# Kernel tuning notes

Measured on AMD Instinct MI355X. Metric: run time of the kernel, lower is better.

## Reference

```python
import jax, jax.numpy as jnp
import numpy as np

N_NODES = 50000
N_EDGES = 400000
IN_DIM = 256
HIDDEN = 256
HEADS = 8
DPH = HIDDEN // HEADS  # 32, out_per_head
OUT_DIM = 128
SEG_EPS = 1e-12   # eps in _segment_softmax
BN_EPS = 1e-5     # torch BatchNorm1d default eps


def _xavier(key, shape):
    fan_in, fan_out = shape[0], shape[-1]
    lim = np.sqrt(6.0 / (fan_in + fan_out))
    return jax.random.uniform(key, shape, jnp.float32, -lim, lim)


def setup_inputs() -> dict:
    key = jax.random.key(0)
    ks = jax.random.split(key, 16)
    x = jax.random.normal(ks[0], (N_NODES, IN_DIM), jnp.float32)
    edge_index = jax.random.randint(ks[1], (2, N_EDGES), 0, N_NODES, jnp.int64)
    return {
        "x": x,
        "edge_index": edge_index,
        # layer 1
        "W1": _xavier(ks[2], (IN_DIM, HIDDEN)),
        "b1": jnp.zeros((HIDDEN,), jnp.float32),
        "a_l1": _xavier(ks[3], (HEADS, DPH)),
        "a_r1": _xavier(ks[4], (HEADS, DPH)),
        "g1": jnp.ones((HIDDEN,), jnp.float32),
        "be1": jnp.zeros((HIDDEN,), jnp.float32),
        # layer 2
        "W2": _xavier(ks[5], (HIDDEN, HIDDEN)),
        "b2": jnp.zeros((HIDDEN,), jnp.float32),
        "a_l2": _xavier(ks[6], (HEADS, DPH)),
        "a_r2": _xavier(ks[7], (HEADS, DPH)),
        "g2": jnp.ones((HIDDEN,), jnp.float32),
        "be2": jnp.zeros((HIDDEN,), jnp.float32),
        # classification head (mlp_hidden=0 -> single Linear)
        "Wh": _xavier(ks[8], (HIDDEN, OUT_DIM)),
        "bh": jnp.zeros((OUT_DIM,), jnp.float32),
    }


def _attn_aggregate(x_proj, src, dst, a_l, a_r):
    """Multi-head GAT aggregation, vectorized over heads.
    x_proj: [N, hidden]; src/dst: [E] int; a_l/a_r: [heads, dph]."""
    N = x_proj.shape[0]
    H = x_proj.reshape(N, HEADS, DPH)
    # per-node score halves (equivalent to (H[src]*a_l).sum + (H[dst]*a_r).sum)
    s_l = jnp.einsum('nhd,hd->nh', H, a_l)  # [N, heads]
    s_r = jnp.einsum('nhd,hd->nh', H, a_r)
    logits = s_l[src] + s_r[dst]            # [E, heads]
    # segment softmax exactly as the source: unstabilized exp + eps denom
    e = jnp.exp(logits)
    denom = jax.ops.segment_sum(e, dst, num_segments=N)       # [N, heads]
    alpha = e / (denom[dst] + SEG_EPS)                         # [E, heads]
    msg = H[src] * alpha[:, :, None]                           # [E, heads, dph]
    out = jax.ops.segment_sum(msg, dst, num_segments=N)        # [N, heads, dph]
    return out.reshape(N, HEADS * DPH)


def _batchnorm(h, gamma, beta):
    # training-mode BatchNorm1d: batch statistics, biased variance
    mean = h.mean(axis=0)
    var = h.var(axis=0)
    return (h - mean) * jax.lax.rsqrt(var + BN_EPS) * gamma + beta


def reference(x, edge_index, W1, b1, a_l1, a_r1, g1, be1,
              W2, b2, a_l2, a_r2, g2, be2, Wh, bh):
    N = x.shape[0]
    # symmetrize edges + add self loops
    ei = jnp.concatenate([edge_index, edge_index[::-1]], axis=1)
    loops = jnp.arange(N, dtype=ei.dtype)
    src = jnp.concatenate([ei[0], loops])
    dst = jnp.concatenate([ei[1], loops])

    x1 = x @ W1 + b1
    x1 = _attn_aggregate(x1, src, dst, a_l1, a_r1)
    x1 = jax.nn.relu(_batchnorm(x1, g1, be1))  # dropout = identity (eval)

    x2 = x1 @ W2 + b2
    x2 = _attn_aggregate(x2, src, dst, a_l2, a_r2)
    x2 = jax.nn.relu(_batchnorm(x2, g2, be2))

    logits = x2 @ Wh + bh  # [N, out_dim]
    return logits
```

## Files before the change

### kernel.cpp

```cpp
#include <hip/hip_runtime.h>
#include <hip/hip_bf16.h>
#include <math.h>

#define NN   50000
#define NE   400000
#define NE2  (2*NE + NN)
#define DIM  256
#define NH   8
#define NM   (NN*DIM)
#define NBLK 196
#define MPAD 50048

typedef __attribute__((ext_vector_type(8))) short bf16x8;
typedef __attribute__((ext_vector_type(4))) float f32x4;

#define GLOAD16(g, l) __builtin_amdgcn_global_load_lds( \
    (const __attribute__((address_space(1))) void*)(g), \
    (__attribute__((address_space(3))) void*)(l), 16, 0, 0)

__device__ __forceinline__ float b2f(unsigned short u) {
    unsigned int i = ((unsigned int)u) << 16;
    float f; __builtin_memcpy(&f, &i, 4); return f;
}
__device__ __forceinline__ unsigned short f2b(float f) {
    __hip_bfloat16 h = __float2bfloat16(f);
    unsigned short u; __builtin_memcpy(&u, &h, 2); return u;
}

__global__ __launch_bounds__(512) void gemm_bf16_wide(
    const unsigned short* __restrict__ A, const unsigned short* __restrict__ Bt,
    const float* __restrict__ bias, unsigned short* __restrict__ Cb)
{
    __shared__ short ldsA[4][128][8];
    __shared__ short ldsB[4][256][8];
    const int tid  = threadIdx.x;
    const int wave = tid >> 6, lane = tid & 63;
    const int wr = wave >> 2, wc = wave & 3;
    const int l15 = lane & 15, lk = lane >> 4;
    const int row0 = blockIdx.x * 128;

    f32x4 acc[4][4] = {};
    for (int k0 = 0; k0 < 256; k0 += 32) {
        GLOAD16(A + (size_t)(row0 + (tid & 127)) * 256 + k0 + (tid >> 7) * 8,
                &ldsA[tid >> 7][tid & 127][0]);
        #pragma unroll
        for (int c = 0; c < 2; ++c) {
            int idx = c * 512 + tid;
            int ch = idx >> 8, r = idx & 255;
            GLOAD16(Bt + (size_t)r * 256 + k0 + ch * 8, &ldsB[ch][r][0]);
        }
        __syncthreads();
        bf16x8 af[4], bf[4];
        #pragma unroll
        for (int m = 0; m < 4; ++m)
            af[m] = *reinterpret_cast<const bf16x8*>(&ldsA[lk][wr*64 + m*16 + l15][0]);
        #pragma unroll
        for (int n = 0; n < 4; ++n)
            bf[n] = *reinterpret_cast<const bf16x8*>(&ldsB[lk][wc*64 + n*16 + l15][0]);
        #pragma unroll
        for (int m = 0; m < 4; ++m)
            #pragma unroll
            for (int n = 0; n < 4; ++n)
                acc[m][n] = __builtin_amdgcn_mfma_f32_16x16x32_bf16(af[m], bf[n], acc[m][n], 0, 0, 0);
        __syncthreads();
    }
    #pragma unroll
    for (int m = 0; m < 4; ++m) {
        #pragma unroll
        for (int n = 0; n < 4; ++n) {
            int col = wc*64 + n*16 + l15;
            float bv = bias[col];
            #pragma unroll
            for (int r = 0; r < 4; ++r) {
                int row = row0 + wr*64 + m*16 + lk*4 + r;
                Cb[(size_t)row * 256 + col] = f2b(acc[m][n][r] + bv);
            }
        }
    }
}

__global__ __launch_bounds__(256) void gemm_bf16_head(
    const unsigned short* __restrict__ A, const unsigned short* __restrict__ Bt,
    const float* __restrict__ bias, float* __restrict__ C)
{
    __shared__ short ldsA[4][128][8];
    __shared__ short ldsB[4][128][8];
    const int tid  = threadIdx.x;
    const int wave = tid >> 6, lane = tid & 63;
    const int wr = wave >> 1, wc = wave & 1;
    const int l15 = lane & 15, lk = lane >> 4;
    const int row0 = blockIdx.x * 128;

    f32x4 acc[4][4] = {};
    for (int k0 = 0; k0 < 256; k0 += 32) {
        #pragma unroll
        for (int c = 0; c < 2; ++c) {
            int idx = c * 256 + tid;
            int ch = idx >> 7, r = idx & 127;
            GLOAD16(A  + (size_t)(row0 + r) * 256 + k0 + ch * 8, &ldsA[ch][r][0]);
            GLOAD16(Bt + (size_t)r * 256 + k0 + ch * 8, &ldsB[ch][r][0]);
        }
        __syncthreads();
        bf16x8 af[4], bf[4];
        #pragma unroll
        for (int m = 0; m < 4; ++m)
            af[m] = *reinterpret_cast<const bf16x8*>(&ldsA[lk][wr*64 + m*16 + l15][0]);
        #pragma unroll
        for (int n = 0; n < 4; ++n)
            bf[n] = *reinterpret_cast<const bf16x8*>(&ldsB[lk][wc*64 + n*16 + l15][0]);
        #pragma unroll
        for (int m = 0; m < 4; ++m)
            #pragma unroll
            for (int n = 0; n < 4; ++n)
                acc[m][n] = __builtin_amdgcn_mfma_f32_16x16x32_bf16(af[m], bf[n], acc[m][n], 0, 0, 0);
        __syncthreads();
    }
    #pragma unroll
    for (int m = 0; m < 4; ++m) {
        #pragma unroll
        for (int n = 0; n < 4; ++n) {
            int col = wc*64 + n*16 + l15;
            float bv = bias[col];
            #pragma unroll
            for (int r = 0; r < 4; ++r) {
                int row = row0 + wr*64 + m*16 + lk*4 + r;
                if (row < NN) C[(size_t)row * 128 + col] = acc[m][n][r] + bv;
            }
        }
    }
}

__global__ __launch_bounds__(256) void cast_x_bf16(
    const float* __restrict__ x, unsigned short* __restrict__ xb)
{
    int idx = blockIdx.x * 256 + threadIdx.x;
    if (idx >= NM / 4) return;
    float4 v = reinterpret_cast<const float4*>(x)[idx];
    ushort4 o = { f2b(v.x), f2b(v.y), f2b(v.z), f2b(v.w) };
    *reinterpret_cast<ushort4*>(&xb[(size_t)idx * 4]) = o;
}

__global__ __launch_bounds__(256) void cast_wt(
    const float* __restrict__ W, unsigned short* __restrict__ Wt, int K, int Nc)
{
    int i = blockIdx.x * 256 + threadIdx.x;
    if (i >= K * Nc) return;
    int k = i / Nc, n = i - k * Nc;
    Wt[n * K + k] = f2b(W[i]);
}

__global__ __launch_bounds__(256) void gat_scores_bf16(
    const unsigned short* __restrict__ Hb, const float* __restrict__ a_l,
    const float* __restrict__ a_r, float* __restrict__ el,
    float* __restrict__ er)
{
    const int wave = threadIdx.x >> 6;
    const int lane = threadIdx.x & 63;
    const int n = blockIdx.x * 4 + wave;
    if (n >= NN) return;
    const int c = lane * 4;
    const int h = lane >> 3;
    ushort4 hv = *reinterpret_cast<const ushort4*>(&Hb[(size_t)n * DIM + c]);
    float4 al4 = *reinterpret_cast<const float4*>(&a_l[c]);
    float4 ar4 = *reinterpret_cast<const float4*>(&a_r[c]);
    float x0 = b2f(hv.x), x1 = b2f(hv.y), x2 = b2f(hv.z), x3 = b2f(hv.w);
    float pl = x0*al4.x + x1*al4.y + x2*al4.z + x3*al4.w;
    float pr = x0*ar4.x + x1*ar4.y + x2*ar4.z + x3*ar4.w;
    #pragma unroll
    for (int o = 1; o < 8; o <<= 1) {
        pl += __shfl_xor(pl, o, 64);
        pr += __shfl_xor(pr, o, 64);
    }
    if ((lane & 7) == 0) {
        el[n * NH + h] = expf(pl);
        er[n * NH + h] = expf(pr);
    }
}

__device__ __forceinline__ void edge_sd(const int* __restrict__ ei, int e2,
                                        int& s, int& d)
{
    if (e2 < NE)          { s = ei[e2];      d = ei[e2 + NE]; }
    else if (e2 < 2 * NE) { s = ei[e2];      d = ei[e2 - NE]; }
    else                  { s = e2 - 2 * NE; d = s; }
}

__global__ __launch_bounds__(256) void deg_count(const int* __restrict__ ei,
                                                 int* __restrict__ deg)
{
    int e2 = blockIdx.x * 256 + threadIdx.x;
    if (e2 >= NE2) return;
    int s, d;
    edge_sd(ei, e2, s, d);
    atomicAdd(&deg[d], 1);
}

__global__ __launch_bounds__(256) void scan_block_sums(
    const int* __restrict__ deg, int* __restrict__ bsum)
{
    __shared__ int tmp[256];
    const int t = threadIdx.x;
    int i = blockIdx.x * 256 + t;
    tmp[t] = (i < NN) ? deg[i] : 0;
    __syncthreads();
    #pragma unroll
    for (int o = 128; o > 0; o >>= 1) {
        if (t < o) tmp[t] += tmp[t + o];
        __syncthreads();
    }
    if (t == 0) bsum[blockIdx.x] = tmp[0];
}

__global__ void scan_bsum(int* __restrict__ bsum)
{
    __shared__ int tmp[256];
    const int t = threadIdx.x;
    int v = (t < NBLK) ? bsum[t] : 0;
    tmp[t] = v;
    __syncthreads();
    #pragma unroll
    for (int o = 1; o < 256; o <<= 1) {
        int x = (t >= o) ? tmp[t - o] : 0;
        __syncthreads();
        tmp[t] += x;
        __syncthreads();
    }
    bsum[t] = tmp[t] - v;
}

__global__ __launch_bounds__(256) void scan_write(
    const int* __restrict__ deg, const int* __restrict__ bsum,
    int* __restrict__ rowoff)
{
    __shared__ int tmp[256];
    const int t = threadIdx.x;
    int i = blockIdx.x * 256 + t;
    int v = (i < NN) ? deg[i] : 0;
    tmp[t] = v;
    __syncthreads();
    #pragma unroll
    for (int o = 1; o < 256; o <<= 1) {
        int x = (t >= o) ? tmp[t - o] : 0;
        __syncthreads();
        tmp[t] += x;
        __syncthreads();
    }
    if (i <= NN) rowoff[i] = bsum[blockIdx.x] + tmp[t] - v;
}

__global__ __launch_bounds__(256) void csr_fill(
    const int* __restrict__ ei, const int* __restrict__ rowoff,
    int* __restrict__ cursor, int* __restrict__ csr)
{
    int e2 = blockIdx.x * 256 + threadIdx.x;
    if (e2 >= NE2) return;
    int s, d;
    edge_sd(ei, e2, s, d);
    int pos = atomicAdd(&cursor[d], 1);
    csr[rowoff[d] + pos] = s;
}

__global__ __launch_bounds__(256) void gat_aggregate_csr_bf16(
    const int* __restrict__ csr, const int* __restrict__ rowoff,
    const unsigned short* __restrict__ Hb, const float* __restrict__ el,
    const float* __restrict__ er, unsigned short* __restrict__ outb)
{
    const int wid  = (blockIdx.x * 256 + threadIdx.x) >> 6;
    const int lane = threadIdx.x & 63;
    if (wid >= NN) return;
    const int h = lane >> 3;
    const int i0 = rowoff[wid], i1 = rowoff[wid + 1];
    const int c4 = lane * 4;

    float ax0 = 0.f, ay0 = 0.f, az0 = 0.f, aw0 = 0.f, den0 = 0.f;
    float ax1 = 0.f, ay1 = 0.f, az1 = 0.f, aw1 = 0.f, den1 = 0.f;

    int i = i0;
    for (; i + 8 <= i1; i += 8) {
        int s[8]; float e[8]; ushort4 hv[8];
        #pragma unroll
        for (int j = 0; j < 8; ++j) s[j] = csr[i + j];
        #pragma unroll
        for (int j = 0; j < 8; ++j) e[j] = el[s[j] * NH + h];
        #pragma unroll
        for (int j = 0; j < 8; ++j)
            hv[j] = *reinterpret_cast<const ushort4*>(&Hb[(size_t)s[j] * DIM + c4]);
        #pragma unroll
        for (int j = 0; j < 8; j += 2) {
            ax0 = fmaf(b2f(hv[j].x), e[j], ax0); ay0 = fmaf(b2f(hv[j].y), e[j], ay0);
            az0 = fmaf(b2f(hv[j].z), e[j], az0); aw0 = fmaf(b2f(hv[j].w), e[j], aw0);
            den0 += e[j];
            ax1 = fmaf(b2f(hv[j+1].x), e[j+1], ax1); ay1 = fmaf(b2f(hv[j+1].y), e[j+1], ay1);
            az1 = fmaf(b2f(hv[j+1].z), e[j+1], az1); aw1 = fmaf(b2f(hv[j+1].w), e[j+1], aw1);
            den1 += e[j+1];
        }
    }
    for (; i + 2 <= i1; i += 2) {
        int s0 = csr[i], s1 = csr[i + 1];
        float e0 = el[s0 * NH + h], e1 = el[s1 * NH + h];
        ushort4 h0 = *reinterpret_cast<const ushort4*>(&Hb[(size_t)s0 * DIM + c4]);
        ushort4 h1 = *reinterpret_cast<const ushort4*>(&Hb[(size_t)s1 * DIM + c4]);
        ax0 = fmaf(b2f(h0.x), e0, ax0); ay0 = fmaf(b2f(h0.y), e0, ay0);
        az0 = fmaf(b2f(h0.z), e0, az0); aw0 = fmaf(b2f(h0.w), e0, aw0);
        den0 += e0;
        ax1 = fmaf(b2f(h1.x), e1, ax1); ay1 = fmaf(b2f(h1.y), e1, ay1);
        az1 = fmaf(b2f(h1.z), e1, az1); aw1 = fmaf(b2f(h1.w), e1, aw1);
        den1 += e1;
    }
    if (i < i1) {
        int s = csr[i];
        float e = el[s * NH + h];
        ushort4 hv = *reinterpret_cast<const ushort4*>(&Hb[(size_t)s * DIM + c4]);
        ax0 = fmaf(b2f(hv.x), e, ax0); ay0 = fmaf(b2f(hv.y), e, ay0);
        az0 = fmaf(b2f(hv.z), e, az0); aw0 = fmaf(b2f(hv.w), e, aw0);
        den0 += e;
    }
    float ax = ax0 + ax1, ay = ay0 + ay1, az = az0 + az1, aw = aw0 + aw1;
    float den = den0 + den1;
    float erv = er[wid * NH + h];
    float inv = erv / fmaf(den, erv, 1e-12f);
    ushort4 r = { f2b(ax * inv), f2b(ay * inv), f2b(az * inv), f2b(aw * inv) };
    *reinterpret_cast<ushort4*>(&outb[(size_t)wid * DIM + c4]) = r;
}

__global__ __launch_bounds__(256) void bn_partial_bf16(
    const unsigned short* __restrict__ H, float* __restrict__ sums)
{
    const int c = threadIdx.x;
    const int r0 = blockIdx.x * 256;
    const int r1 = min(r0 + 256, NN);
    float s = 0.f, q = 0.f;
    for (int r = r0; r < r1; ++r) {
        float v = b2f(H[(size_t)r * DIM + c]);
        s += v;
        q = fmaf(v, v, q);
    }
    atomicAdd(&sums[c], s);
    atomicAdd(&sums[DIM + c], q);
}

__global__ __launch_bounds__(256) void bn_apply_relu_bf16(
    const unsigned short* __restrict__ in, const float* __restrict__ sums,
    const float* __restrict__ g, const float* __restrict__ be,
    unsigned short* __restrict__ out)
{
    __shared__ float sc[DIM], sh[DIM];
    const int t = threadIdx.x;
    {
        float mean = sums[t] * (1.f / NN);
        float var  = sums[DIM + t] * (1.f / NN) - mean * mean;
        float s    = g[t] * rsqrtf(var + 1e-5f);
        sc[t] = s;
        sh[t] = be[t] - mean * s;
    }
    __syncthreads();
    int idx = blockIdx.x * 256 + t;
    if (idx >= NM / 4) return;
    int c4 = (idx & 63) * 4;
    ushort4 v = reinterpret_cast<const ushort4*>(in)[idx];
    ushort4 r = {
        f2b(fmaxf(0.f, fmaf(b2f(v.x), sc[c4 + 0], sh[c4 + 0]))),
        f2b(fmaxf(0.f, fmaf(b2f(v.y), sc[c4 + 1], sh[c4 + 1]))),
        f2b(fmaxf(0.f, fmaf(b2f(v.z), sc[c4 + 2], sh[c4 + 2]))),
        f2b(fmaxf(0.f, fmaf(b2f(v.w), sc[c4 + 3], sh[c4 + 3]))) };
    reinterpret_cast<ushort4*>(out)[idx] = r;
}

extern "C" void kernel_launch(void* const* d_in, const int* in_sizes, int n_in,
                              void* d_out, int out_size, void* d_ws, size_t ws_size,
                              hipStream_t stream)
{
    const float* x   = (const float*)d_in[0];
    const int*   ei  = (const int*)  d_in[1];
    const float* W1  = (const float*)d_in[2];
    const float* b1  = (const float*)d_in[3];
    const float* al1 = (const float*)d_in[4];
    const float* ar1 = (const float*)d_in[5];
    const float* g1  = (const float*)d_in[6];
    const float* be1 = (const float*)d_in[7];
    const float* W2  = (const float*)d_in[8];
    const float* b2  = (const float*)d_in[9];
    const float* al2 = (const float*)d_in[10];
    const float* ar2 = (const float*)d_in[11];
    const float* g2  = (const float*)d_in[12];
    const float* be2 = (const float*)d_in[13];
    const float* Wh  = (const float*)d_in[14];
    const float* bh  = (const float*)d_in[15];
    float* out = (float*)d_out;

    float* ws     = (float*)d_ws;
    float* el     = ws;
    float* er     = el + NN * NH;
    float* bnsum1 = er + NN * NH;
    float* bnsum2 = bnsum1 + 2 * DIM;
    int*   deg    = (int*)(bnsum2 + 2 * DIM);
    int*   cursor = deg + NN;
    int*   rowoff = cursor + NN;
    int*   bsum   = rowoff + NN + 1;
    int*   csr    = bsum + 256;
    unsigned short* xb =
        (unsigned short*)((((uintptr_t)(csr + NE2)) + 63) & ~(uintptr_t)63);
    unsigned short* Hb  = xb  + (size_t)MPAD * 256;
    unsigned short* Ab  = Hb  + (size_t)MPAD * 256;
    unsigned short* Wt1 = Ab  + (size_t)NN * 256;
    unsigned short* Wt2 = Wt1 + 256 * 256;
    unsigned short* Wth = Wt2 + 256 * 256;

    const int gemmBlocks  = MPAD / 128;
    const int edgeBlocks  = (NE2 + 255) / 256;
    const int nodeBlocks  = (NN * 64 + 255) / 256;
    const int bnpBlocks   = (NN + 255) / 256;
    const int elemBlocks  = NM / 4 / 256;

    cast_wt<<<(256 * 256 + 255) / 256, 256, 0, stream>>>(W1, Wt1, 256, 256);
    cast_wt<<<(256 * 256 + 255) / 256, 256, 0, stream>>>(W2, Wt2, 256, 256);
    cast_wt<<<(256 * 128 + 255) / 256, 256, 0, stream>>>(Wh, Wth, 256, 128);
    cast_x_bf16<<<elemBlocks, 256, 0, stream>>>(x, xb);

    hipMemsetAsync(deg, 0, 2 * NN * sizeof(int), stream);
    hipMemsetAsync(bnsum1, 0, 4 * DIM * sizeof(float), stream);

    deg_count<<<edgeBlocks, 256, 0, stream>>>(ei, deg);
    scan_block_sums<<<NBLK, 256, 0, stream>>>(deg, bsum);
    scan_bsum<<<1, 256, 0, stream>>>(bsum);
    scan_write<<<NBLK, 256, 0, stream>>>(deg, bsum, rowoff);
    csr_fill<<<edgeBlocks, 256, 0, stream>>>(ei, rowoff, cursor, csr);

    gemm_bf16_wide<<<gemmBlocks, 512, 0, stream>>>(xb, Wt1, b1, Hb);
    gat_scores_bf16<<<nodeBlocks, 256, 0, stream>>>(Hb, al1, ar1, el, er);
    gat_aggregate_csr_bf16<<<nodeBlocks, 256, 0, stream>>>(csr, rowoff, Hb, el, er, Ab);
    bn_partial_bf16<<<bnpBlocks, 256, 0, stream>>>(Ab, bnsum1);
    bn_apply_relu_bf16<<<elemBlocks, 256, 0, stream>>>(Ab, bnsum1, g1, be1, xb);

    gemm_bf16_wide<<<gemmBlocks, 512, 0, stream>>>(xb, Wt2, b2, Hb);
    gat_scores_bf16<<<nodeBlocks, 256, 0, stream>>>(Hb, al2, ar2, el, er);
    gat_aggregate_csr_bf16<<<nodeBlocks, 256, 0, stream>>>(csr, rowoff, Hb, el, er, Ab);
    bn_partial_bf16<<<bnpBlocks, 256, 0, stream>>>(Ab, bnsum2);
    bn_apply_relu_bf16<<<elemBlocks, 256, 0, stream>>>(Ab, bnsum2, g2, be2, xb);

    gemm_bf16_head<<<gemmBlocks, 256, 0, stream>>>(xb, Wth, bh, out);
}
```

Baseline: 502.2 us.

## Double-buffer GEMM LDS tiles, fuse weight casts, shrink aggregate unroll

```diff
diff --git a/kernel.cpp b/kernel.cpp
--- a/kernel.cpp
+++ b/kernel.cpp
@@ -31,38 +31,60 @@
     const unsigned short* __restrict__ A, const unsigned short* __restrict__ Bt,
     const float* __restrict__ bias, unsigned short* __restrict__ Cb)
 {
-    __shared__ short ldsA[4][128][8];
-    __shared__ short ldsB[4][256][8];
+    __shared__ short ldsA[2][4][128][8];
+    __shared__ short ldsB[2][4][256][8];
     const int tid  = threadIdx.x;
     const int wave = tid >> 6, lane = tid & 63;
     const int wr = wave >> 2, wc = wave & 3;
     const int l15 = lane & 15, lk = lane >> 4;
     const int row0 = blockIdx.x * 128;
 
-    f32x4 acc[4][4] = {};
-    for (int k0 = 0; k0 < 256; k0 += 32) {
+    auto STAGE = [&](int b, int k0) {
         GLOAD16(A + (size_t)(row0 + (tid & 127)) * 256 + k0 + (tid >> 7) * 8,
-                &ldsA[tid >> 7][tid & 127][0]);
+                &ldsA[b][tid >> 7][tid & 127][0]);
         #pragma unroll
         for (int c = 0; c < 2; ++c) {
             int idx = c * 512 + tid;
             int ch = idx >> 8, r = idx & 255;
-            GLOAD16(Bt + (size_t)r * 256 + k0 + ch * 8, &ldsB[ch][r][0]);
+            GLOAD16(Bt + (size_t)r * 256 + k0 + ch * 8, &ldsB[b][ch][r][0]);
         }
-        __syncthreads();
+    };
+
+    f32x4 acc[4][4] = {};
+    STAGE(0, 0);
+    __syncthreads();
+    int cur = 0;
+    #pragma unroll
+    for (int t = 0; t < 7; ++t) {
+        STAGE(cur ^ 1, (t + 1) * 32);
         bf16x8 af[4], bf[4];
         #pragma unroll
         for (int m = 0; m < 4; ++m)
-            af[m] = *reinterpret_cast<const bf16x8*>(&ldsA[lk][wr*64 + m*16 + l15][0]);
+            af[m] = *reinterpret_cast<const bf16x8*>(&ldsA[cur][lk][wr*64 + m*16 + l15][0]);
         #pragma unroll
         for (int n = 0; n < 4; ++n)
-            bf[n] = *reinterpret_cast<const bf16x8*>(&ldsB[lk][wc*64 + n*16 + l15][0]);
+            bf[n] = *reinterpret_cast<const bf16x8*>(&ldsB[cur][lk][wc*64 + n*16 + l15][0]);
         #pragma unroll
         for (int m = 0; m < 4; ++m)
             #pragma unroll
             for (int n = 0; n < 4; ++n)
                 acc[m][n] = __builtin_amdgcn_mfma_f32_16x16x32_bf16(af[m], bf[n], acc[m][n], 0, 0, 0);
         __syncthreads();
+        cur ^= 1;
+    }
+    {
+        bf16x8 af[4], bf[4];
+        #pragma unroll
+        for (int m = 0; m < 4; ++m)
+            af[m] = *reinterpret_cast<const bf16x8*>(&ldsA[cur][lk][wr*64 + m*16 + l15][0]);
+        #pragma unroll
+        for (int n = 0; n < 4; ++n)
+            bf[n] = *reinterpret_cast<const bf16x8*>(&ldsB[cur][lk][wc*64 + n*16 + l15][0]);
+        #pragma unroll
+        for (int m = 0; m < 4; ++m)
+            #pragma unroll
+            for (int n = 0; n < 4; ++n)
+                acc[m][n] = __builtin_amdgcn_mfma_f32_16x16x32_bf16(af[m], bf[n], acc[m][n], 0, 0, 0);
     }
     #pragma unroll
     for (int m = 0; m < 4; ++m) {
@@ -83,37 +105,59 @@
     const unsigned short* __restrict__ A, const unsigned short* __restrict__ Bt,
     const float* __restrict__ bias, float* __restrict__ C)
 {
-    __shared__ short ldsA[4][128][8];
-    __shared__ short ldsB[4][128][8];
+    __shared__ short ldsA[2][4][128][8];
+    __shared__ short ldsB[2][4][128][8];
     const int tid  = threadIdx.x;
     const int wave = tid >> 6, lane = tid & 63;
     const int wr = wave >> 1, wc = wave & 1;
     const int l15 = lane & 15, lk = lane >> 4;
     const int row0 = blockIdx.x * 128;
 
-    f32x4 acc[4][4] = {};
-    for (int k0 = 0; k0 < 256; k0 += 32) {
+    auto STAGE = [&](int b, int k0) {
         #pragma unroll
         for (int c = 0; c < 2; ++c) {
             int idx = c * 256 + tid;
             int ch = idx >> 7, r = idx & 127;
-            GLOAD16(A  + (size_t)(row0 + r) * 256 + k0 + ch * 8, &ldsA[ch][r][0]);
-            GLOAD16(Bt + (size_t)r * 256 + k0 + ch * 8, &ldsB[ch][r][0]);
+            GLOAD16(A  + (size_t)(row0 + r) * 256 + k0 + ch * 8, &ldsA[b][ch][r][0]);
+            GLOAD16(Bt + (size_t)r * 256 + k0 + ch * 8, &ldsB[b][ch][r][0]);
         }
-        __syncthreads();
+    };
+
+    f32x4 acc[4][4] = {};
+    STAGE(0, 0);
+    __syncthreads();
+    int cur = 0;
+    #pragma unroll
+    for (int t = 0; t < 7; ++t) {
+        STAGE(cur ^ 1, (t + 1) * 32);
         bf16x8 af[4], bf[4];
         #pragma unroll
         for (int m = 0; m < 4; ++m)
-            af[m] = *reinterpret_cast<const bf16x8*>(&ldsA[lk][wr*64 + m*16 + l15][0]);
+            af[m] = *reinterpret_cast<const bf16x8*>(&ldsA[cur][lk][wr*64 + m*16 + l15][0]);
         #pragma unroll
         for (int n = 0; n < 4; ++n)
-            bf[n] = *reinterpret_cast<const bf16x8*>(&ldsB[lk][wc*64 + n*16 + l15][0]);
+            bf[n] = *reinterpret_cast<const bf16x8*>(&ldsB[cur][lk][wc*64 + n*16 + l15][0]);
         #pragma unroll
         for (int m = 0; m < 4; ++m)
             #pragma unroll
             for (int n = 0; n < 4; ++n)
                 acc[m][n] = __builtin_amdgcn_mfma_f32_16x16x32_bf16(af[m], bf[n], acc[m][n], 0, 0, 0);
         __syncthreads();
+        cur ^= 1;
+    }
+    {
+        bf16x8 af[4], bf[4];
+        #pragma unroll
+        for (int m = 0; m < 4; ++m)
+            af[m] = *reinterpret_cast<const bf16x8*>(&ldsA[cur][lk][wr*64 + m*16 + l15][0]);
+        #pragma unroll
+        for (int n = 0; n < 4; ++n)
+            bf[n] = *reinterpret_cast<const bf16x8*>(&ldsB[cur][lk][wc*64 + n*16 + l15][0]);
+        #pragma unroll
+        for (int m = 0; m < 4; ++m)
+            #pragma unroll
+            for (int n = 0; n < 4; ++n)
+                acc[m][n] = __builtin_amdgcn_mfma_f32_16x16x32_bf16(af[m], bf[n], acc[m][n], 0, 0, 0);
     }
     #pragma unroll
     for (int m = 0; m < 4; ++m) {
@@ -140,13 +184,21 @@
     *reinterpret_cast<ushort4*>(&xb[(size_t)idx * 4]) = o;
 }
 
-__global__ __launch_bounds__(256) void cast_wt(
-    const float* __restrict__ W, unsigned short* __restrict__ Wt, int K, int Nc)
+__global__ __launch_bounds__(256) void cast_wt_all(
+    const float* __restrict__ W1, const float* __restrict__ W2,
+    const float* __restrict__ Wh, unsigned short* __restrict__ Wt1,
+    unsigned short* __restrict__ Wt2, unsigned short* __restrict__ Wth)
 {
     int i = blockIdx.x * 256 + threadIdx.x;
-    if (i >= K * Nc) return;
-    int k = i / Nc, n = i - k * Nc;
-    Wt[n * K + k] = f2b(W[i]);
+    {
+        int k = i >> 8, n = i & 255;
+        Wt1[n * 256 + k] = f2b(W1[i]);
+        Wt2[n * 256 + k] = f2b(W2[i]);
+    }
+    if (i < 256 * 128) {
+        int k = i >> 7, n = i & 127;
+        Wth[n * 256 + k] = f2b(Wh[i]);
+    }
 }
 
 __global__ __launch_bounds__(256) void gat_scores_bf16(
@@ -276,38 +328,28 @@
     float ax1 = 0.f, ay1 = 0.f, az1 = 0.f, aw1 = 0.f, den1 = 0.f;
 
     int i = i0;
-    for (; i + 8 <= i1; i += 8) {
-        int s[8]; float e[8]; ushort4 hv[8];
-        #pragma unroll
-        for (int j = 0; j < 8; ++j) s[j] = csr[i + j];
-        #pragma unroll
-        for (int j = 0; j < 8; ++j) e[j] = el[s[j] * NH + h];
-        #pragma unroll
-        for (int j = 0; j < 8; ++j)
-            hv[j] = *reinterpret_cast<const ushort4*>(&Hb[(size_t)s[j] * DIM + c4]);
-        #pragma unroll
-        for (int j = 0; j < 8; j += 2) {
-            ax0 = fmaf(b2f(hv[j].x), e[j], ax0); ay0 = fmaf(b2f(hv[j].y), e[j], ay0);
-            az0 = fmaf(b2f(hv[j].z), e[j], az0); aw0 = fmaf(b2f(hv[j].w), e[j], aw0);
-            den0 += e[j];
-            ax1 = fmaf(b2f(hv[j+1].x), e[j+1], ax1); ay1 = fmaf(b2f(hv[j+1].y), e[j+1], ay1);
-            az1 = fmaf(b2f(hv[j+1].z), e[j+1], az1); aw1 = fmaf(b2f(hv[j+1].w), e[j+1], aw1);
-            den1 += e[j+1];
-        }
-    }
-    for (; i + 2 <= i1; i += 2) {
-        int s0 = csr[i], s1 = csr[i + 1];
+    for (; i + 4 <= i1; i += 4) {
+        int s0 = csr[i + 0], s1 = csr[i + 1], s2 = csr[i + 2], s3 = csr[i + 3];
         float e0 = el[s0 * NH + h], e1 = el[s1 * NH + h];
+        float e2 = el[s2 * NH + h], e3 = el[s3 * NH + h];
         ushort4 h0 = *reinterpret_cast<const ushort4*>(&Hb[(size_t)s0 * DIM + c4]);
         ushort4 h1 = *reinterpret_cast<const ushort4*>(&Hb[(size_t)s1 * DIM + c4]);
+        ushort4 h2 = *reinterpret_cast<const ushort4*>(&Hb[(size_t)s2 * DIM + c4]);
+        ushort4 h3 = *reinterpret_cast<const ushort4*>(&Hb[(size_t)s3 * DIM + c4]);
         ax0 = fmaf(b2f(h0.x), e0, ax0); ay0 = fmaf(b2f(h0.y), e0, ay0);
         az0 = fmaf(b2f(h0.z), e0, az0); aw0 = fmaf(b2f(h0.w), e0, aw0);
         den0 += e0;
         ax1 = fmaf(b2f(h1.x), e1, ax1); ay1 = fmaf(b2f(h1.y), e1, ay1);
         az1 = fmaf(b2f(h1.z), e1, az1); aw1 = fmaf(b2f(h1.w), e1, aw1);
         den1 += e1;
-    }
-    if (i < i1) {
+        ax0 = fmaf(b2f(h2.x), e2, ax0); ay0 = fmaf(b2f(h2.y), e2, ay0);
+        az0 = fmaf(b2f(h2.z), e2, az0); aw0 = fmaf(b2f(h2.w), e2, aw0);
+        den0 += e2;
+        ax1 = fmaf(b2f(h3.x), e3, ax1); ay1 = fmaf(b2f(h3.y), e3, ay1);
+        az1 = fmaf(b2f(h3.z), e3, az1); aw1 = fmaf(b2f(h3.w), e3, aw1);
+        den1 += e3;
+    }
+    for (; i < i1; ++i) {
         int s = csr[i];
         float e = el[s * NH + h];
         ushort4 hv = *reinterpret_cast<const ushort4*>(&Hb[(size_t)s * DIM + c4]);
@@ -412,9 +454,7 @@
     const int bnpBlocks   = (NN + 255) / 256;
     const int elemBlocks  = NM / 4 / 256;
 
-    cast_wt<<<(256 * 256 + 255) / 256, 256, 0, stream>>>(W1, Wt1, 256, 256);
-    cast_wt<<<(256 * 256 + 255) / 256, 256, 0, stream>>>(W2, Wt2, 256, 256);
-    cast_wt<<<(256 * 128 + 255) / 256, 256, 0, stream>>>(Wh, Wth, 256, 128);
+    cast_wt_all<<<256, 256, 0, stream>>>(W1, W2, Wh, Wt1, Wt2, Wth);
     cast_x_bf16<<<elemBlocks, 256, 0, stream>>>(x, xb);
 
     hipMemsetAsync(deg, 0, 2 * NN * sizeof(int), stream);
```

Result: no change. 502.6 us (+0.1%).
